# Kernel optimization log

Hardware: AMD Instinct MI355X
Metric: run time of the kernel (lower is better)

The kernel has to match this reference:

```python
import jax, jax.numpy as jnp
import numpy as np

B, C, H, W = 32, 3, 512, 512
PCT = 3.0  # normalization_percentile_threshold
D0 = int(max(0.5 * min(H, W) // 2, 1))  # = 128


def _build_filter_map():
    # cv2.rectangle(thickness=-1) fills inclusive of both corner points, clipped to image
    f = np.zeros((H, W), dtype=np.float32)
    f[:D0 + 1, :D0 + 1] = 1.0
    f[:D0 + 1, W - D0:] = 1.0
    f[H - D0:, :D0 + 1] = 1.0
    f[H - D0:, W - D0:] = 1.0
    return jnp.asarray(f)


def setup_inputs() -> dict:
    key = jax.random.key(0)
    k1, k2 = jax.random.split(key)
    x = jax.random.normal(k1, (B, C, H, W), dtype=jnp.float32)
    # binary field-of-view mask, broadcastable over channels
    mask = (jax.random.uniform(k2, (B, 1, H, W)) > 0.2).astype(jnp.float32)
    return {"x": x, "mask": mask, "filter_map": _build_filter_map()}


def _median_padding(x, mask):
    b, c, h, w = x.shape
    # torch.median returns the LOWER of the two middle values for even counts
    flat = x.reshape(b, c, h * w)
    med = jnp.sort(flat, axis=-1)[..., (h * w - 1) // 2] + 0.2  # [B, C]
    med = med[:, :, None, None]
    return mask * x + (1.0 - mask) * med


def reference(x, mask, filter_map):
    x = _median_padding(x, mask)
    # FFT2 over last two dims, corner-keep frequency mask, magnitude of ifft2
    res = jnp.abs(jnp.fft.ifft2(jnp.fft.fft2(x) * filter_map))
    b, c, h, w = res.shape
    # quantize as (res*256).int().float()/256  -> truncation toward zero
    q = jnp.trunc(res * 256.0) / 256.0
    qf = q.reshape(b, c, h * w)
    lo = jnp.percentile(qf, PCT, axis=-1)          # [B, C]
    hi = jnp.percentile(qf, 100.0 - PCT, axis=-1)  # [B, C]
    res = (res - lo[:, :, None, None]) / (hi - lo)[:, :, None, None]
    return res * mask  # sub_mask=True
```

## Files before the change

### kernel.cpp

```cpp
#include <hip/hip_runtime.h>
#include <math.h>

#define HW 262144
#define NIMG 96
#define NQBIN 4096

typedef __attribute__((ext_vector_type(8))) short bf16x8;
typedef __attribute__((ext_vector_type(4))) float f32x4;

__device__ __forceinline__ unsigned fmap_u(float f){
  unsigned u = __float_as_uint(f);
  return (u & 0x80000000u) ? ~u : (u | 0x80000000u);
}
__device__ __forceinline__ float funmap_u(unsigned u){
  unsigned v = (u & 0x80000000u) ? (u & 0x7fffffffu) : ~u;
  return __uint_as_float(v);
}
__device__ __forceinline__ unsigned bf16rne(float f){
  unsigned u = __float_as_uint(f);
  return (u + 0x7fffu + ((u >> 16) & 1u)) >> 16;
}

typedef __attribute__((address_space(3))) unsigned lds_u;
typedef const __attribute__((address_space(1))) unsigned glb_u;
__device__ __forceinline__ void gll16(const void* g, void* l){
  __builtin_amdgcn_global_load_lds((glb_u*)g, (lds_u*)l, 16, 0, 0);
}

__global__ void k_dir(const float* __restrict__ fmap_in, float* __restrict__ Dir){
  int n = blockIdx.x;
  int t = threadIdx.x;
  double s = 0.0;
  for(int c = t; c < 512; c += 256){
    int a = (c * n) & 511;
    s += (double)fmap_in[c] * cos(6.283185307179586476925287 * (double)a / 512.0);
  }
  __shared__ double red[256];
  red[t] = s; __syncthreads();
  for(int off = 128; off; off >>= 1){
    if(t < off) red[t] += red[t + off];
    __syncthreads();
  }
  if(t == 0) Dir[n] = (float)(red[0] / 512.0);
}

__global__ void k_cmat(const float* __restrict__ Dir, unsigned short* __restrict__ CmH){
  int a = blockIdx.x;
  for(int b = threadIdx.x; b < 512; b += 256){
    float d = Dir[(a - b) & 511];
    CmH[(size_t)a * 512 + b] = (unsigned short)bf16rne(d);
  }
}

__global__ __launch_bounds__(256) void k_p1(const float* __restrict__ x, unsigned* __restrict__ h){
  __shared__ unsigned sh[2][4112];
  const int img  = blockIdx.x >> 3;
  const int part = blockIdx.x & 7;
  const int par  = threadIdx.x & 1;
  const float4* p = (const float4*)(x + (size_t)img * HW + (size_t)part * 32768);
  for(int i = threadIdx.x; i < 4112; i += 256){ sh[0][i] = 0; sh[1][i] = 0; }
  __syncthreads();
  unsigned* mine = sh[par];
  for(int i = threadIdx.x; i < 8192; i += 256){
    float4 v = p[i];
    atomicAdd(&mine[fmap_u(v.x) >> 20], 1u);
    atomicAdd(&mine[fmap_u(v.y) >> 20], 1u);
    atomicAdd(&mine[fmap_u(v.z) >> 20], 1u);
    atomicAdd(&mine[fmap_u(v.w) >> 20], 1u);
  }
  __syncthreads();
  unsigned* hh = h + (size_t)img * 4096;
  for(int i = threadIdx.x; i < 4096; i += 256){
    unsigned c = sh[0][i] + sh[1][i];
    if(c) atomicAdd(&hh[i], c);
  }
}

__global__ void k_med12(const unsigned* __restrict__ h, float* __restrict__ med){
  int img = blockIdx.x, t = threadIdx.x;
  const unsigned* hh = h + (size_t)img * 4096;
  __shared__ unsigned csum[256];
  unsigned s = 0;
  for(int j = 0; j < 16; j++) s += hh[t * 16 + j];
  csum[t] = s; __syncthreads();
  if(t == 0){
    unsigned k = 131071u, cum = 0; int chunk = 0;
    for(; chunk < 256; ++chunk){ if(cum + csum[chunk] > k) break; cum += csum[chunk]; }
    int b = chunk * 16;
    unsigned c;
    for(;; ++b){ c = hh[b]; if(cum + c > k) break; cum += c; }
    float frac = ((float)(k - cum) + 0.5f) / (float)c;
    unsigned m = ((unsigned)b << 20) + (unsigned)(frac * 1048576.0f);
    med[img] = funmap_u(m) + 0.2f;
  }
}

__global__ __launch_bounds__(512, 4) void k_rowpass(
    const float* __restrict__ x, const float* __restrict__ mask,
    const float* __restrict__ med,
    const unsigned short* __restrict__ CmH,
    unsigned short* __restrict__ t1h)
{
  __shared__ __align__(16) unsigned short As [2][8192];
  __shared__ __align__(16) unsigned short BsH[2][8192];

  const int b    = blockIdx.x;
  const int xcd  = b & 7;
  const int i8   = b >> 3;
  const int rblk = xcd * 48 + (i8 >> 2);
  const int nblk = i8 & 3;
  const int r0 = rblk * 128;
  const int n0 = nblk * 128;
  const int bc = r0 >> 9;
  const int bb = bc / 3;
  const float mv = med[bc];

  const int t    = threadIdx.x;
  const int lane = t & 63;
  const int wv   = t >> 6;
  const int wm   = (wv >> 2) * 64;
  const int wn   = (wv & 3) * 32;
  const int fr   = lane & 15;
  const int fg   = lane >> 4;
  const int sw   = lane & 7;

  const int srow = t >> 2;
  const int sc   = (t & 3) << 4;
  const float* xr = x    + ((size_t)(r0 + srow) << 9) + sc;
  const float* mr = mask + (size_t)bb * HW + ((size_t)((r0 + srow) & 511) << 9) + sc;

  const int drow = lane >> 3;
  const int dblk = (lane & 7) ^ drow;
  const unsigned short* bhsrc = CmH + ((size_t)(n0 + wv*8 + drow) << 9) + dblk * 8;
  const int dbase = wv * 8 * 64;

  f32x4 acc[4][2];
  #pragma unroll
  for(int i = 0; i < 4; i++)
    #pragma unroll
    for(int j = 0; j < 2; j++) acc[i][j] = (f32x4){0.f, 0.f, 0.f, 0.f};

  float4 px[4], pm[4];

  auto ALOAD = [&](int k0){
    #pragma unroll
    for(int q = 0; q < 4; q++){
      px[q] = *(const float4*)(xr + k0 + q * 4);
      pm[q] = *(const float4*)(mr + k0 + q * 4);
    }
  };
  auto BDMA = [&](int buf, int k0){
    #pragma unroll
    for(int q = 0; q < 2; q++){
      const size_t so = ((size_t)(q * 64) << 9) + k0;
      const int    dq = dbase + q * 4096;
      gll16(bhsrc + so, &BsH[buf][dq]);
    }
  };
  auto ACONV = [&](int buf){
    unsigned hp[8];
    #pragma unroll
    for(int q = 0; q < 4; q++){
      unsigned h0 = bf16rne((pm[q].x != 0.f) ? px[q].x : mv);
      unsigned h1 = bf16rne((pm[q].y != 0.f) ? px[q].y : mv);
      unsigned h2 = bf16rne((pm[q].z != 0.f) ? px[q].z : mv);
      unsigned h3 = bf16rne((pm[q].w != 0.f) ? px[q].w : mv);
      hp[q*2]   = (h1 << 16) | h0;
      hp[q*2+1] = (h3 << 16) | h2;
    }
    const int b0 = (t & 3) * 2;
    *(uint4*)&As[buf][srow * 64 + (( b0      ^ (srow & 7)) << 3)] = make_uint4(hp[0], hp[1], hp[2], hp[3]);
    *(uint4*)&As[buf][srow * 64 + (((b0 | 1) ^ (srow & 7)) << 3)] = make_uint4(hp[4], hp[5], hp[6], hp[7]);
  };
  auto COMPUTE = [&](int buf){
    bf16x8 af[4][2], bh[2][2];
    #pragma unroll
    for(int i = 0; i < 4; i++)
      #pragma unroll
      for(int kq = 0; kq < 2; kq++){
        int row = wm + i*16 + fr;
        af[i][kq] = *(const bf16x8*)&As[buf][row*64 + (((kq*4 + fg) ^ sw) << 3)];
      }
    #pragma unroll
    for(int j = 0; j < 2; j++)
      #pragma unroll
      for(int kq = 0; kq < 2; kq++){
        int row = wn + j*16 + fr;
        bh[j][kq] = *(const bf16x8*)&BsH[buf][row*64 + (((kq*4 + fg) ^ sw) << 3)];
      }
    __builtin_amdgcn_s_setprio(1);
    #pragma unroll
    for(int i = 0; i < 4; i++)
      #pragma unroll
      for(int j = 0; j < 2; j++){
        acc[i][j] = __builtin_amdgcn_mfma_f32_16x16x32_bf16(af[i][0], bh[j][0], acc[i][j], 0, 0, 0);
        acc[i][j] = __builtin_amdgcn_mfma_f32_16x16x32_bf16(af[i][1], bh[j][1], acc[i][j], 0, 0, 0);
      }
    __builtin_amdgcn_s_setprio(0);
  };

  ALOAD(0); BDMA(0, 0);
  asm volatile("s_waitcnt vmcnt(2)" ::: "memory");
  ACONV(0);
  asm volatile("s_waitcnt vmcnt(0) lgkmcnt(0)" ::: "memory");
  __builtin_amdgcn_sched_barrier(0);
  __builtin_amdgcn_s_barrier();

  #pragma unroll
  for(int it = 0; it < 7; ++it){
    ALOAD((it + 1) * 64);
    BDMA((it + 1) & 1, (it + 1) * 64);
    COMPUTE(it & 1);
    asm volatile("s_waitcnt vmcnt(2)" ::: "memory");
    ACONV((it + 1) & 1);
    asm volatile("s_waitcnt vmcnt(0) lgkmcnt(0)" ::: "memory");
    __builtin_amdgcn_sched_barrier(0);
    __builtin_amdgcn_s_barrier();
  }
  COMPUTE(1);

  const int img = r0 >> 9;
  const int hb  = r0 & 511;
  #pragma unroll
  for(int i = 0; i < 4; i++)
    #pragma unroll
    for(int j = 0; j < 2; j++){
      f32x4 a = acc[i][j];
      unsigned b0 = bf16rne(a[0]), b1 = bf16rne(a[1]), b2 = bf16rne(a[2]), b3 = bf16rne(a[3]);
      int n = n0 + wn + j*16 + fr;
      int h = hb + wm + i*16 + fg*4;
      *(uint2*)&t1h[(size_t)img * HW + ((size_t)n << 9) + h] =
          make_uint2((b1<<16)|b0, (b3<<16)|b2);
    }
}

__global__ __launch_bounds__(512, 4) void k_colpass(
    const unsigned short* __restrict__ t1h,
    const unsigned short* __restrict__ CmH,
    unsigned short* __restrict__ resh, unsigned* __restrict__ qh)
{
  __shared__ __align__(16) unsigned short AsH[2][8192];
  __shared__ __align__(16) unsigned short Bs [2][8192];

  const int b    = blockIdx.x;
  const int xcd  = b & 7;
  const int i8   = b >> 3;
  const int img  = xcd * 12 + (i8 >> 4);
  const int r16  = i8 & 15;
  const int hp0  = (r16 >> 2) * 128;
  const int w0   = (r16 & 3) * 128;

  const int t    = threadIdx.x;
  const int lane = t & 63;
  const int wv   = t >> 6;
  const int wm   = (wv >> 2) * 64;
  const int wn   = (wv & 3) * 32;
  const int fr   = lane & 15;
  const int fg   = lane >> 4;
  const int sw   = lane & 7;

  const int drow = lane >> 3;
  const int dblk = (lane & 7) ^ drow;
  const unsigned short* ahsrc = CmH + ((size_t)(hp0 + wv*8 + drow) << 9) + dblk * 8;
  const unsigned short* bsrc  = t1h + (size_t)img * HW + ((size_t)(w0 + wv*8 + drow) << 9) + dblk * 8;
  const int dbase = wv * 8 * 64;

  f32x4 acc[4][2];
  #pragma unroll
  for(int i = 0; i < 4; i++)
    #pragma unroll
    for(int j = 0; j < 2; j++) acc[i][j] = (f32x4){0.f, 0.f, 0.f, 0.f};

  auto STAGE = [&](int buf, int k0){
    #pragma unroll
    for(int q = 0; q < 2; q++){
      const size_t so = ((size_t)(q * 64) << 9) + k0;
      const int    dq = dbase + q * 4096;
      gll16(ahsrc + so, &AsH[buf][dq]);
      gll16(bsrc  + so, &Bs [buf][dq]);
    }
  };
  auto COMPUTE = [&](int buf){
    bf16x8 ah[4][2], bv[2][2];
    #pragma unroll
    for(int i = 0; i < 4; i++)
      #pragma unroll
      for(int kq = 0; kq < 2; kq++){
        int row = wm + i*16 + fr;
        ah[i][kq] = *(const bf16x8*)&AsH[buf][row*64 + (((kq*4 + fg) ^ sw) << 3)];
      }
    #pragma unroll
    for(int j = 0; j < 2; j++)
      #pragma unroll
      for(int kq = 0; kq < 2; kq++){
        int row = wn + j*16 + fr;
        bv[j][kq] = *(const bf16x8*)&Bs[buf][row*64 + (((kq*4 + fg) ^ sw) << 3)];
      }
    __builtin_amdgcn_s_setprio(1);
    #pragma unroll
    for(int i = 0; i < 4; i++)
      #pragma unroll
      for(int j = 0; j < 2; j++){
        acc[i][j] = __builtin_amdgcn_mfma_f32_16x16x32_bf16(ah[i][0], bv[j][0], acc[i][j], 0, 0, 0);
        acc[i][j] = __builtin_amdgcn_mfma_f32_16x16x32_bf16(ah[i][1], bv[j][1], acc[i][j], 0, 0, 0);
      }
    __builtin_amdgcn_s_setprio(0);
  };

  STAGE(0, 0);
  asm volatile("s_waitcnt vmcnt(0)" ::: "memory");
  __builtin_amdgcn_s_barrier();
  #pragma unroll
  for(int it = 0; it < 7; ++it){
    STAGE((it + 1) & 1, (it + 1) * 64);
    asm volatile("s_waitcnt vmcnt(4)" ::: "memory");
    __builtin_amdgcn_s_barrier();
    COMPUTE(it & 1);
    asm volatile("" ::: "memory");
    __builtin_amdgcn_s_barrier();
  }
  asm volatile("s_waitcnt vmcnt(0)" ::: "memory");
  __builtin_amdgcn_s_barrier();
  COMPUTE(1);

  __syncthreads();
  unsigned* shh = (unsigned*)&AsH[0][0];
  for(int i = t; i < NQBIN; i += 512) shh[i] = 0;
  __syncthreads();

  unsigned short* rimg = resh + (size_t)img * HW;
  #pragma unroll
  for(int i = 0; i < 4; i++)
    #pragma unroll
    for(int j = 0; j < 2; j++){
      f32x4 a = acc[i][j];
      int w  = w0 + wn + j*16 + fr;
      int hp = hp0 + wm + i*16 + fg*4;
      #pragma unroll
      for(int r = 0; r < 4; r++){
        float v = fabsf(a[r]);
        rimg[((size_t)(hp + r) << 9) + w] = (unsigned short)bf16rne(v);
        atomicAdd(&shh[min((int)(v * 256.f), NQBIN - 1)], 1u);
      }
    }
  __syncthreads();

  unsigned* hg = qh + (size_t)img * NQBIN;
  for(int i = t; i < NQBIN; i += 512){
    unsigned c = shh[i];
    if(c) atomicAdd(&hg[i], c);
  }
}

__global__ void k_pct(const unsigned* __restrict__ qh, float2* __restrict__ prm){
  int img = blockIdx.x, t = threadIdx.x;
  const unsigned* h = qh + (size_t)img * NQBIN;
  __shared__ unsigned sh[NQBIN];
  for(int i = t; i < NQBIN; i += 256) sh[i] = h[i];
  __syncthreads();
  if(t == 0){
    const unsigned targ[4] = {7864u, 7865u, 254278u, 254279u};
    float v[4]; unsigned cum = 0; int b = 0;
    for(int q = 0; q < 4; q++){
      while(cum + sh[b] <= targ[q]){ cum += sh[b]; ++b; }
      v[q] = (float)b * (1.0f / 256.0f);
    }
    double plo = 0.03 * 262143.0;
    double phi = 0.97 * 262143.0;
    float lo = v[0] + (float)(plo - 7864.0)   * (v[1] - v[0]);
    float hi = v[2] + (float)(phi - 254278.0) * (v[3] - v[2]);
    prm[img] = make_float2(lo, 1.0f / (hi - lo));
  }
}

__global__ __launch_bounds__(256) void k_norm(const unsigned short* __restrict__ resh,
                                              const float* __restrict__ mask,
                                              const float2* __restrict__ prm,
                                              float* __restrict__ out){
  size_t i8 = (size_t)blockIdx.x * blockDim.x + threadIdx.x;
  const size_t total8 = (size_t)NIMG * HW / 8;
  const size_t step = (size_t)gridDim.x * blockDim.x;
  for(; i8 < total8; i8 += step){
    size_t i = i8 * 8;
    int bc = (int)(i >> 18);
    int bb = bc / 3;
    size_t mi = ((size_t)bb << 18) + (i & 0x3FFFFu);
    uint4 rv = *(const uint4*)(resh + i);
    float4 m0 = *(const float4*)(mask + mi);
    float4 m1 = *(const float4*)(mask + mi + 4);
    float2 p = prm[bc];
    float4 o0, o1;
    o0.x = (__uint_as_float((rv.x & 0xFFFFu) << 16) - p.x) * p.y * m0.x;
    o0.y = (__uint_as_float((rv.x & 0xFFFF0000u))   - p.x) * p.y * m0.y;
    o0.z = (__uint_as_float((rv.y & 0xFFFFu) << 16) - p.x) * p.y * m0.z;
    o0.w = (__uint_as_float((rv.y & 0xFFFF0000u))   - p.x) * p.y * m0.w;
    o1.x = (__uint_as_float((rv.z & 0xFFFFu) << 16) - p.x) * p.y * m1.x;
    o1.y = (__uint_as_float((rv.z & 0xFFFF0000u))   - p.x) * p.y * m1.y;
    o1.z = (__uint_as_float((rv.w & 0xFFFFu) << 16) - p.x) * p.y * m1.z;
    o1.w = (__uint_as_float((rv.w & 0xFFFF0000u))   - p.x) * p.y * m1.w;
    *(float4*)(out + i)     = o0;
    *(float4*)(out + i + 4) = o1;
  }
}

extern "C" void kernel_launch(void* const* d_in, const int* in_sizes, int n_in,
                              void* d_out, int out_size, void* d_ws, size_t ws_size,
                              hipStream_t stream)
{
  const float* x       = (const float*)d_in[0];
  const float* mask    = (const float*)d_in[1];
  const float* fmap_in = (const float*)d_in[2];
  float* out = (float*)d_out;

  const size_t T1_BYTES = (size_t)NIMG * HW * 2;
  const size_t QH_BYTES = (size_t)NIMG * NQBIN * 4;
  char* ws = (char*)d_ws;
  unsigned short* t1h  = (unsigned short*)ws;
  unsigned*       qh   = (unsigned*)(ws + T1_BYTES);
  unsigned short* resh = (unsigned short*)(ws + T1_BYTES + QH_BYTES);
  unsigned* h1 = (unsigned*)ws;
  char* tail = ws + 2 * T1_BYTES + QH_BYTES;
  float*          Dir = (float*)tail;
  unsigned short* CmH = (unsigned short*)(tail + 2048);
  char* tail2 = tail + 2048 + 524288;
  float*  med  = (float*)tail2;
  float2* prm  = (float2*)(tail2 + 512);

  k_dir<<<512, 256, 0, stream>>>(fmap_in, Dir);
  k_cmat<<<512, 256, 0, stream>>>(Dir, CmH);

  hipMemsetAsync(h1, 0, (size_t)NIMG * 4096 * 4, stream);
  k_p1<<<NIMG * 8, 256, 0, stream>>>(x, h1);
  k_med12<<<NIMG, 256, 0, stream>>>(h1, med);

  hipMemsetAsync(qh, 0, QH_BYTES, stream);
  k_rowpass<<<1536, 512, 0, stream>>>(x, mask, med, CmH, t1h);
  k_colpass<<<1536, 512, 0, stream>>>(t1h, CmH, resh, qh);

  k_pct<<<NIMG, 256, 0, stream>>>(qh, prm);
  k_norm<<<2048, 256, 0, stream>>>(resh, mask, prm, out);
}
```

Measured before the change: 216.4 us.

## Precompute padded bf16 input and stage row-pass A tiles via direct LDS loads

Adds a pre-pass kernel that applies the median padding and converts the input to bf16 once. The row-pass GEMM then loads its A tiles with direct global-to-LDS copies instead of loading fp32 x and mask per tile and converting in registers. This removes the repeated fp32 x/mask reads (one per column block) and the in-loop conversion, at the cost of an extra kernel launch and a 50 MB intermediate write and read. The padded buffer reuses the result buffer's workspace.

```diff
diff --git a/kernel.cpp b/kernel.cpp
--- a/kernel.cpp
+++ b/kernel.cpp
@@ -95,9 +95,32 @@
   }
 }
 
+__global__ __launch_bounds__(256) void k_prepad(
+    const float* __restrict__ x, const float* __restrict__ mask,
+    const float* __restrict__ med, unsigned short* __restrict__ xh)
+{
+  size_t u8 = (size_t)blockIdx.x * 256 + threadIdx.x;
+  size_t i  = u8 * 8;
+  int img = (int)(i >> 18);
+  size_t mi = ((size_t)(img / 3) << 18) + (i & 0x3FFFFu);
+  const float mv = med[img];
+  unsigned hp[4];
+  #pragma unroll
+  for(int q = 0; q < 2; q++){
+    float4 xv = *(const float4*)(x + i + q * 4);
+    float4 mk = *(const float4*)(mask + mi + q * 4);
+    unsigned h0 = bf16rne((mk.x != 0.f) ? xv.x : mv);
+    unsigned h1 = bf16rne((mk.y != 0.f) ? xv.y : mv);
+    unsigned h2 = bf16rne((mk.z != 0.f) ? xv.z : mv);
+    unsigned h3 = bf16rne((mk.w != 0.f) ? xv.w : mv);
+    hp[q*2]   = (h1 << 16) | h0;
+    hp[q*2+1] = (h3 << 16) | h2;
+  }
+  *(uint4*)(xh + i) = make_uint4(hp[0], hp[1], hp[2], hp[3]);
+}
+
 __global__ __launch_bounds__(512, 4) void k_rowpass(
-    const float* __restrict__ x, const float* __restrict__ mask,
-    const float* __restrict__ med,
+    const unsigned short* __restrict__ xh,
     const unsigned short* __restrict__ CmH,
     unsigned short* __restrict__ t1h)
 {
@@ -111,9 +134,6 @@
   const int nblk = i8 & 3;
   const int r0 = rblk * 128;
   const int n0 = nblk * 128;
-  const int bc = r0 >> 9;
-  const int bb = bc / 3;
-  const float mv = med[bc];
 
   const int t    = threadIdx.x;
   const int lane = t & 63;
@@ -124,13 +144,9 @@
   const int fg   = lane >> 4;
   const int sw   = lane & 7;
 
-  const int srow = t >> 2;
-  const int sc   = (t & 3) << 4;
-  const float* xr = x    + ((size_t)(r0 + srow) << 9) + sc;
-  const float* mr = mask + (size_t)bb * HW + ((size_t)((r0 + srow) & 511) << 9) + sc;
-
   const int drow = lane >> 3;
   const int dblk = (lane & 7) ^ drow;
+  const unsigned short* asrc  = xh  + ((size_t)(r0 + wv*8 + drow) << 9) + dblk * 8;
   const unsigned short* bhsrc = CmH + ((size_t)(n0 + wv*8 + drow) << 9) + dblk * 8;
   const int dbase = wv * 8 * 64;
 
@@ -140,38 +156,15 @@
     #pragma unroll
     for(int j = 0; j < 2; j++) acc[i][j] = (f32x4){0.f, 0.f, 0.f, 0.f};
 
-  float4 px[4], pm[4];
-
-  auto ALOAD = [&](int k0){
-    #pragma unroll
-    for(int q = 0; q < 4; q++){
-      px[q] = *(const float4*)(xr + k0 + q * 4);
-      pm[q] = *(const float4*)(mr + k0 + q * 4);
-    }
-  };
-  auto BDMA = [&](int buf, int k0){
+  auto STAGE = [&](int buf, int k0){
     #pragma unroll
     for(int q = 0; q < 2; q++){
       const size_t so = ((size_t)(q * 64) << 9) + k0;
       const int    dq = dbase + q * 4096;
+      gll16(asrc  + so, &As [buf][dq]);
       gll16(bhsrc + so, &BsH[buf][dq]);
     }
   };
-  auto ACONV = [&](int buf){
-    unsigned hp[8];
-    #pragma unroll
-    for(int q = 0; q < 4; q++){
-      unsigned h0 = bf16rne((pm[q].x != 0.f) ? px[q].x : mv);
-      unsigned h1 = bf16rne((pm[q].y != 0.f) ? px[q].y : mv);
-      unsigned h2 = bf16rne((pm[q].z != 0.f) ? px[q].z : mv);
-      unsigned h3 = bf16rne((pm[q].w != 0.f) ? px[q].w : mv);
-      hp[q*2]   = (h1 << 16) | h0;
-      hp[q*2+1] = (h3 << 16) | h2;
-    }
-    const int b0 = (t & 3) * 2;
-    *(uint4*)&As[buf][srow * 64 + (( b0      ^ (srow & 7)) << 3)] = make_uint4(hp[0], hp[1], hp[2], hp[3]);
-    *(uint4*)&As[buf][srow * 64 + (((b0 | 1) ^ (srow & 7)) << 3)] = make_uint4(hp[4], hp[5], hp[6], hp[7]);
-  };
   auto COMPUTE = [&](int buf){
     bf16x8 af[4][2], bh[2][2];
     #pragma unroll
@@ -199,24 +192,20 @@
     __builtin_amdgcn_s_setprio(0);
   };
 
-  ALOAD(0); BDMA(0, 0);
-  asm volatile("s_waitcnt vmcnt(2)" ::: "memory");
-  ACONV(0);
-  asm volatile("s_waitcnt vmcnt(0) lgkmcnt(0)" ::: "memory");
-  __builtin_amdgcn_sched_barrier(0);
+  STAGE(0, 0);
+  asm volatile("s_waitcnt vmcnt(0)" ::: "memory");
   __builtin_amdgcn_s_barrier();
-
   #pragma unroll
   for(int it = 0; it < 7; ++it){
-    ALOAD((it + 1) * 64);
-    BDMA((it + 1) & 1, (it + 1) * 64);
+    STAGE((it + 1) & 1, (it + 1) * 64);
+    asm volatile("s_waitcnt vmcnt(4)" ::: "memory");
+    __builtin_amdgcn_s_barrier();
     COMPUTE(it & 1);
-    asm volatile("s_waitcnt vmcnt(2)" ::: "memory");
-    ACONV((it + 1) & 1);
-    asm volatile("s_waitcnt vmcnt(0) lgkmcnt(0)" ::: "memory");
-    __builtin_amdgcn_sched_barrier(0);
+    asm volatile("" ::: "memory");
     __builtin_amdgcn_s_barrier();
   }
+  asm volatile("s_waitcnt vmcnt(0)" ::: "memory");
+  __builtin_amdgcn_s_barrier();
   COMPUTE(1);
 
   const int img = r0 >> 9;
@@ -417,7 +406,8 @@
   char* ws = (char*)d_ws;
   unsigned short* t1h  = (unsigned short*)ws;
   unsigned*       qh   = (unsigned*)(ws + T1_BYTES);
-  unsigned short* resh = (unsigned short*)(ws + T1_BYTES + QH_BYTES);
+  unsigned short* xh   = (unsigned short*)(ws + T1_BYTES + QH_BYTES);
+  unsigned short* resh = xh;
   unsigned* h1 = (unsigned*)ws;
   char* tail = ws + 2 * T1_BYTES + QH_BYTES;
   float*          Dir = (float*)tail;
@@ -433,8 +423,10 @@
   k_p1<<<NIMG * 8, 256, 0, stream>>>(x, h1);
   k_med12<<<NIMG, 256, 0, stream>>>(h1, med);
 
+  k_prepad<<<(NIMG * HW / 8) / 256, 256, 0, stream>>>(x, mask, med, xh);
+
   hipMemsetAsync(qh, 0, QH_BYTES, stream);
-  k_rowpass<<<1536, 512, 0, stream>>>(x, mask, med, CmH, t1h);
+  k_rowpass<<<1536, 512, 0, stream>>>(xh, CmH, t1h);
   k_colpass<<<1536, 512, 0, stream>>>(t1h, CmH, resh, qh);
 
   k_pct<<<NIMG, 256, 0, stream>>>(qh, prm);
```

Result: faster. 195.9 us (-9.5%).
